# Performance work log

Measured on AMD Instinct MI355X. Metric: run time of the kernel, lower is better.

The kernel has to match this reference:

```python
import jax, jax.numpy as jnp
import numpy as np


def setup_inputs() -> dict:
    key = jax.random.key(0)
    k1, k2, k3 = jax.random.split(key, 3)
    B, F, N = 8, 16, 2048
    # strictly positive features so momentum.log() is finite
    emb = jax.random.uniform(k1, (B, F, N), dtype=jnp.float32, minval=1e-3, maxval=1.0)
    # torch init: alpha * (rand(1,1)*0.02 + 0.99), beta * (rand(1,1,1)*0.02 + 0.99)
    alpha_p = 1.0 * (jax.random.uniform(k2, (1, 1), dtype=jnp.float32) * 0.02 + 0.99)
    beta_p = 1.0 * (jax.random.uniform(k3, (1, 1, 1), dtype=jnp.float32) * 0.02 + 0.99)
    return {"emb": emb, "alpha_p": alpha_p, "beta_p": beta_p}


def reference(emb, alpha_p, beta_p):
    # emb: [B, F, N]
    # pairwise squared distances over the feature dim:
    # sqdist[b,i,j] = ||e[:, i] - e[:, j]||^2 = n_i + n_j - 2 * <e_i, e_j>
    sq_norms = jnp.sum(emb * emb, axis=1)                 # [B, N]
    gram = jnp.einsum('bfi,bfj->bij', emb, emb)           # [B, N, N]
    sqdist = sq_norms[:, :, None] + sq_norms[:, None, :] - 2.0 * gram

    momentum = emb[:, 4, :]                               # [B, N]
    alpha = alpha_p[0, 0]                                 # scalar broadcast
    pow_momenta = jnp.exp(2.0 * alpha * jnp.log(momentum))  # momentum ** (2*alpha)
    # sym_min: min(p_i, p_j) pairwise -> [B, N, N]
    min_momenta = jnp.minimum(pow_momenta[:, :, None], pow_momenta[:, None, :])

    d_ij = sqdist * min_momenta                           # [B, N, N]
    # NOTE: _renorm in the source is computed then discarded (overwritten);
    # faithful math uses d_ij directly.
    beta_sq = beta_p[0, 0, 0] ** 2
    w_ij = jnp.exp(-beta_sq * d_ij)                       # [B, N, N]
    return w_ij
```

## Files before the change

kernel.cpp:

```cpp
#include <hip/hip_runtime.h>


#define BATCH 8
#define FDIM 16
#define NPT 2048
#define TILE 128

__global__ __launch_bounds__(256, 4) void qcd_aware_kernel(
    const float* __restrict__ emb,
    const float* __restrict__ alpha_p,
    const float* __restrict__ beta_p,
    float* __restrict__ out)
{
    __shared__ float As[FDIM][TILE];
    __shared__ float Bs[FDIM][TILE];
    __shared__ float nI[TILE], nJ[TILE], qI[TILE], qJ[TILE];

    const int b  = blockIdx.z;
    const int i0 = blockIdx.y * TILE;
    const int j0 = blockIdx.x * TILE;
    const int tid = threadIdx.x;

    {
        float* AsF = &As[0][0];
        float* BsF = &Bs[0][0];
        const float* base = emb + (size_t)b * FDIM * NPT;
        #pragma unroll
        for (int r = 0; r < 4; ++r) {
            const int w = 2 * tid + 512 * r;
            const int f = w >> 7;
            const int i = w & 127;
            *(float2*)&AsF[w] = *(const float2*)(base + (size_t)f * NPT + i0 + i);
            *(float2*)&BsF[w] = *(const float2*)(base + (size_t)f * NPT + j0 + i);
        }
    }
    __syncthreads();

    const float alpha2 = 2.0f * alpha_p[0];
    const float beta   = beta_p[0];
    const float qscale = -(beta * beta) * 1.4426950408889634f;

    {
        const int e = tid & 127;
        float s = 0.f;
        if (tid < TILE) {
            #pragma unroll
            for (int f = 0; f < FDIM; ++f) { float v = As[f][e]; s += v * v; }
            nI[e] = s;
            qI[e] = qscale * __expf(alpha2 * __logf(As[4][e]));
        } else {
            #pragma unroll
            for (int f = 0; f < FDIM; ++f) { float v = Bs[f][e]; s += v * v; }
            nJ[e] = s;
            qJ[e] = qscale * __expf(alpha2 * __logf(Bs[4][e]));
        }
    }
    __syncthreads();

    const int tx4 = (tid & 15) * 4;
    const int ty4 = (tid >> 4) * 4;

    float acc[8][8] = {};
    #pragma unroll
    for (int f = 0; f < FDIM; ++f) {
        const float4 a0 = *(const float4*)&As[f][ty4];
        const float4 a1 = *(const float4*)&As[f][ty4 + 64];
        const float4 b0 = *(const float4*)&Bs[f][tx4];
        const float4 b1 = *(const float4*)&Bs[f][tx4 + 64];
        const float av[8] = {a0.x, a0.y, a0.z, a0.w, a1.x, a1.y, a1.z, a1.w};
        const float bv[8] = {b0.x, b0.y, b0.z, b0.w, b1.x, b1.y, b1.z, b1.w};
        #pragma unroll
        for (int ii = 0; ii < 8; ++ii)
            #pragma unroll
            for (int jj = 0; jj < 8; ++jj)
                acc[ii][jj] = fmaf(av[ii], bv[jj], acc[ii][jj]);
    }

    float nj[8], qj[8];
    #pragma unroll
    for (int jj = 0; jj < 4; ++jj) {
        nj[jj]     = nJ[tx4 + jj];      qj[jj]     = qJ[tx4 + jj];
        nj[jj + 4] = nJ[tx4 + 64 + jj]; qj[jj + 4] = qJ[tx4 + 64 + jj];
    }

    #pragma unroll
    for (int ih = 0; ih < 2; ++ih) {
        #pragma unroll
        for (int ii = 0; ii < 4; ++ii) {
            const int il = ih * 64 + ty4 + ii;
            const float ni = nI[il];
            const float qi = qI[il];
            const size_t rowp = ((size_t)b * NPT + (size_t)(i0 + il)) * NPT + j0;
            #pragma unroll
            for (int jh = 0; jh < 2; ++jh) {
                float4 w;
                float* wv = (float*)&w;
                #pragma unroll
                for (int jj = 0; jj < 4; ++jj) {
                    const int jr = jh * 4 + jj;
                    const float s = ni + nj[jr];
                    const float d = fmaf(-2.0f, acc[ih * 4 + ii][jh * 4 + jj], s);
                    wv[jj] = __builtin_amdgcn_exp2f(fmaxf(qi, qj[jr]) * d);
                }
                *(float4*)(out + rowp + jh * 64 + tx4) = w;
            }
        }
    }
}

extern "C" void kernel_launch(void* const* d_in, const int* in_sizes, int n_in,
                              void* d_out, int out_size, void* d_ws, size_t ws_size,
                              hipStream_t stream) {
    const float* emb     = (const float*)d_in[0];
    const float* alpha_p = (const float*)d_in[1];
    const float* beta_p  = (const float*)d_in[2];
    float* out = (float*)d_out;

    dim3 grid(NPT / TILE, NPT / TILE, BATCH);
    dim3 block(256);
    qcd_aware_kernel<<<grid, block, 0, stream>>>(emb, alpha_p, beta_p, out);
}
```

Measured before the change: 142.1 us.

## Exploit output symmetry by computing upper-triangle tiles and writing both halves

The grid now launches only upper-triangular tile pairs per batch. Each block computes its tile once and stores it both at its own position and, transposed, at the mirrored position. This is meant to remove the redundant Gram and exp work for the symmetric half of the matrix. The kernel is dominated by output writes, so total bytes written stay the same, and it adds fewer, more imbalanced blocks plus transposed float4 stores that are less coalesced.

```diff
diff --git a/kernel.cpp b/kernel.cpp
--- a/kernel.cpp
+++ b/kernel.cpp
@@ -5,6 +5,8 @@
 #define FDIM 16
 #define NPT 2048
 #define TILE 128
+#define NT (NPT / TILE)
+#define NPAIRS (NT * (NT + 1) / 2)
 
 __global__ __launch_bounds__(256, 4) void qcd_aware_kernel(
     const float* __restrict__ emb,
@@ -16,9 +18,14 @@
     __shared__ float Bs[FDIM][TILE];
     __shared__ float nI[TILE], nJ[TILE], qI[TILE], qJ[TILE];
 
-    const int b  = blockIdx.z;
-    const int i0 = blockIdx.y * TILE;
-    const int j0 = blockIdx.x * TILE;
+    const int b = blockIdx.y;
+
+    int t  = blockIdx.x;
+    int ti = 0;
+    while (t >= NT - ti) { t -= NT - ti; ++ti; }
+    const int tj = ti + t;
+    const int i0 = ti * TILE;
+    const int j0 = tj * TILE;
     const int tid = threadIdx.x;
 
     {
@@ -84,25 +91,40 @@
     }
 
     #pragma unroll
-    for (int ih = 0; ih < 2; ++ih) {
+    for (int r = 0; r < 8; ++r) {
+        const int il = (r >> 2) * 64 + ty4 + (r & 3);
+        const float ni = nI[il];
+        const float qi = qI[il];
         #pragma unroll
-        for (int ii = 0; ii < 4; ++ii) {
-            const int il = ih * 64 + ty4 + ii;
-            const float ni = nI[il];
-            const float qi = qI[il];
-            const size_t rowp = ((size_t)b * NPT + (size_t)(i0 + il)) * NPT + j0;
+        for (int c = 0; c < 8; ++c) {
+            const float s = ni + nj[c];
+            const float d = fmaf(-2.0f, acc[r][c], s);
+            acc[r][c] = __builtin_amdgcn_exp2f(fmaxf(qi, qj[c]) * d);
+        }
+    }
+
+    #pragma unroll
+    for (int r = 0; r < 8; ++r) {
+        const int il = (r >> 2) * 64 + ty4 + (r & 3);
+        const size_t rowp = ((size_t)b * NPT + (size_t)(i0 + il)) * NPT + j0;
+        #pragma unroll
+        for (int jh = 0; jh < 2; ++jh) {
+            const float4 w = make_float4(acc[r][jh * 4 + 0], acc[r][jh * 4 + 1],
+                                         acc[r][jh * 4 + 2], acc[r][jh * 4 + 3]);
+            *(float4*)(out + rowp + jh * 64 + tx4) = w;
+        }
+    }
+
+    if (ti != tj) {
+        #pragma unroll
+        for (int c = 0; c < 8; ++c) {
+            const int jl = (c >> 2) * 64 + tx4 + (c & 3);
+            const size_t rowp = ((size_t)b * NPT + (size_t)(j0 + jl)) * NPT + i0;
             #pragma unroll
-            for (int jh = 0; jh < 2; ++jh) {
-                float4 w;
-                float* wv = (float*)&w;
-                #pragma unroll
-                for (int jj = 0; jj < 4; ++jj) {
-                    const int jr = jh * 4 + jj;
-                    const float s = ni + nj[jr];
-                    const float d = fmaf(-2.0f, acc[ih * 4 + ii][jh * 4 + jj], s);
-                    wv[jj] = __builtin_amdgcn_exp2f(fmaxf(qi, qj[jr]) * d);
-                }
-                *(float4*)(out + rowp + jh * 64 + tx4) = w;
+            for (int ih = 0; ih < 2; ++ih) {
+                const float4 w = make_float4(acc[ih * 4 + 0][c], acc[ih * 4 + 1][c],
+                                             acc[ih * 4 + 2][c], acc[ih * 4 + 3][c]);
+                *(float4*)(out + rowp + ih * 64 + ty4) = w;
             }
         }
     }
@@ -116,7 +138,7 @@
     const float* beta_p  = (const float*)d_in[2];
     float* out = (float*)d_out;
 
-    dim3 grid(NPT / TILE, NPT / TILE, BATCH);
+    dim3 grid(NPAIRS, BATCH);
     dim3 block(256);
     qcd_aware_kernel<<<grid, block, 0, stream>>>(emb, alpha_p, beta_p, out);
 }
```

Measured after the change: 143.9 us. About the same (+1.3%).

## Retile to wide 32x1024 tiles with 512 threads for contiguous row stores

Applied to the files above, without the earlier changes.

Changes the output tile from 128x128 to 32 rows by 1024 columns with 512-thread blocks. Each wavefront now owns four full rows and writes 256-float contiguous segments, which should improve write coalescing on this output-bandwidth-bound kernel. The cost is recomputing column norms and powers over a much wider tile per block and loading 64KB of shared data, which may limit occupancy. Per-thread accumulators drop to 4x16.

```diff
diff --git a/kernel.cpp b/kernel.cpp
--- a/kernel.cpp
+++ b/kernel.cpp
@@ -4,34 +4,42 @@
 #define BATCH 8
 #define FDIM 16
 #define NPT 2048
-#define TILE 128
+#define TI 32
+#define TJ 1024
+#define NTHREADS 512
 
-__global__ __launch_bounds__(256, 4) void qcd_aware_kernel(
+__global__ __launch_bounds__(NTHREADS, 4) void qcd_aware_kernel(
     const float* __restrict__ emb,
     const float* __restrict__ alpha_p,
     const float* __restrict__ beta_p,
     float* __restrict__ out)
 {
-    __shared__ float As[FDIM][TILE];
-    __shared__ float Bs[FDIM][TILE];
-    __shared__ float nI[TILE], nJ[TILE], qI[TILE], qJ[TILE];
+    __shared__ float Bs[FDIM][TJ];
+    __shared__ float Af[FDIM][TI];
+    __shared__ float nJ[TJ], qJ[TJ];
+    __shared__ float nI[TI], qI[TI];
 
     const int b  = blockIdx.z;
-    const int i0 = blockIdx.y * TILE;
-    const int j0 = blockIdx.x * TILE;
-    const int tid = threadIdx.x;
+    const int i0 = blockIdx.y * TI;
+    const int j0 = blockIdx.x * TJ;
+    const int t  = threadIdx.x;
+
+    const float* base = emb + (size_t)b * FDIM * NPT;
 
     {
-        float* AsF = &As[0][0];
         float* BsF = &Bs[0][0];
-        const float* base = emb + (size_t)b * FDIM * NPT;
         #pragma unroll
-        for (int r = 0; r < 4; ++r) {
-            const int w = 2 * tid + 512 * r;
-            const int f = w >> 7;
-            const int i = w & 127;
-            *(float2*)&AsF[w] = *(const float2*)(base + (size_t)f * NPT + i0 + i);
-            *(float2*)&BsF[w] = *(const float2*)(base + (size_t)f * NPT + j0 + i);
+        for (int g = 0; g < 8; ++g) {
+            const int w = 4 * t + 2048 * g;
+            const int f = w >> 10;
+            const int j = w & 1023;
+            *(float4*)&BsF[w] = *(const float4*)(base + (size_t)f * NPT + j0 + j);
+        }
+        if (t < 128) {
+            const int w = 4 * t;
+            const int f = w >> 5;
+            const int i = w & 31;
+            *(float4*)(&Af[0][0] + w) = *(const float4*)(base + (size_t)f * NPT + i0 + i);
         }
     }
     __syncthreads();
@@ -41,69 +49,65 @@
     const float qscale = -(beta * beta) * 1.4426950408889634f;
 
     {
-        const int e = tid & 127;
-        float s = 0.f;
-        if (tid < TILE) {
+        #pragma unroll
+        for (int g = 0; g < 2; ++g) {
+            const int c = t + NTHREADS * g;
+            float s = 0.f;
             #pragma unroll
-            for (int f = 0; f < FDIM; ++f) { float v = As[f][e]; s += v * v; }
-            nI[e] = s;
-            qI[e] = qscale * __expf(alpha2 * __logf(As[4][e]));
-        } else {
+            for (int f = 0; f < FDIM; ++f) { float v = Bs[f][c]; s += v * v; }
+            nJ[c] = s;
+            qJ[c] = qscale * __expf(alpha2 * __logf(Bs[4][c]));
+        }
+        if (t < TI) {
+            float s = 0.f;
             #pragma unroll
-            for (int f = 0; f < FDIM; ++f) { float v = Bs[f][e]; s += v * v; }
-            nJ[e] = s;
-            qJ[e] = qscale * __expf(alpha2 * __logf(Bs[4][e]));
+            for (int f = 0; f < FDIM; ++f) { float v = Af[f][t]; s += v * v; }
+            nI[t] = s;
+            qI[t] = qscale * __expf(alpha2 * __logf(Af[4][t]));
         }
     }
     __syncthreads();
 
-    const int tx4 = (tid & 15) * 4;
-    const int ty4 = (tid >> 4) * 4;
+    const int wv  = t >> 6;
+    const int r0  = 4 * wv;
+    const int tx4 = (t & 63) * 4;
 
-    float acc[8][8] = {};
+    float acc[4][16] = {};
     #pragma unroll
     for (int f = 0; f < FDIM; ++f) {
-        const float4 a0 = *(const float4*)&As[f][ty4];
-        const float4 a1 = *(const float4*)&As[f][ty4 + 64];
-        const float4 b0 = *(const float4*)&Bs[f][tx4];
-        const float4 b1 = *(const float4*)&Bs[f][tx4 + 64];
-        const float av[8] = {a0.x, a0.y, a0.z, a0.w, a1.x, a1.y, a1.z, a1.w};
-        const float bv[8] = {b0.x, b0.y, b0.z, b0.w, b1.x, b1.y, b1.z, b1.w};
+        const float4 a = *(const float4*)&Af[f][r0];
+        const float av[4] = {a.x, a.y, a.z, a.w};
         #pragma unroll
-        for (int ii = 0; ii < 8; ++ii)
+        for (int g = 0; g < 4; ++g) {
+            const float4 bq = *(const float4*)&Bs[f][tx4 + 256 * g];
+            const float bb[4] = {bq.x, bq.y, bq.z, bq.w};
             #pragma unroll
-            for (int jj = 0; jj < 8; ++jj)
-                acc[ii][jj] = fmaf(av[ii], bv[jj], acc[ii][jj]);
-    }
-
-    float nj[8], qj[8];
-    #pragma unroll
-    for (int jj = 0; jj < 4; ++jj) {
-        nj[jj]     = nJ[tx4 + jj];      qj[jj]     = qJ[tx4 + jj];
-        nj[jj + 4] = nJ[tx4 + 64 + jj]; qj[jj + 4] = qJ[tx4 + 64 + jj];
+            for (int ii = 0; ii < 4; ++ii)
+                #pragma unroll
+                for (int jj = 0; jj < 4; ++jj)
+                    acc[ii][g * 4 + jj] = fmaf(av[ii], bb[jj], acc[ii][g * 4 + jj]);
+        }
     }
 
     #pragma unroll
-    for (int ih = 0; ih < 2; ++ih) {
+    for (int g = 0; g < 4; ++g) {
+        const float4 njv = *(const float4*)&nJ[tx4 + 256 * g];
+        const float4 qjv = *(const float4*)&qJ[tx4 + 256 * g];
+        const float nj[4] = {njv.x, njv.y, njv.z, njv.w};
+        const float qj[4] = {qjv.x, qjv.y, qjv.z, qjv.w};
         #pragma unroll
         for (int ii = 0; ii < 4; ++ii) {
-            const int il = ih * 64 + ty4 + ii;
-            const float ni = nI[il];
-            const float qi = qI[il];
-            const size_t rowp = ((size_t)b * NPT + (size_t)(i0 + il)) * NPT + j0;
+            const float ni = nI[r0 + ii];
+            const float qi = qI[r0 + ii];
+            float4 wo;
+            float* wp = (float*)&wo;
             #pragma unroll
-            for (int jh = 0; jh < 2; ++jh) {
-                float4 w;
-                float* wv = (float*)&w;
-                #pragma unroll
-                for (int jj = 0; jj < 4; ++jj) {
-                    const int jr = jh * 4 + jj;
-                    const float s = ni + nj[jr];
-                    const float d = fmaf(-2.0f, acc[ih * 4 + ii][jh * 4 + jj], s);
-                    wv[jj] = __builtin_amdgcn_exp2f(fmaxf(qi, qj[jr]) * d);
-                }
-                *(float4*)(out + rowp + jh * 64 + tx4) = w;
+            for (int jj = 0; jj < 4; ++jj) {
+                const float d = fmaf(-2.0f, acc[ii][g * 4 + jj], ni + nj[jj]);
+                wp[jj] = __builtin_amdgcn_exp2f(fmaxf(qi, qj[jj]) * d);
             }
+            const size_t rowp = ((size_t)b * NPT + (size_t)(i0 + r0 + ii)) * NPT + j0;
+            *(float4*)(out + rowp + tx4 + 256 * g) = wo;
         }
     }
 }
@@ -116,7 +120,7 @@
     const float* beta_p  = (const float*)d_in[2];
     float* out = (float*)d_out;
 
-    dim3 grid(NPT / TILE, NPT / TILE, BATCH);
-    dim3 block(256);
+    dim3 grid(NPT / TJ, NPT / TI, BATCH);
+    dim3 block(NTHREADS);
     qcd_aware_kernel<<<grid, block, 0, stream>>>(emb, alpha_p, beta_p, out);
 }
```

Result: slower. 148.5 us (+4.5%).
